# Kernel optimization log

Hardware: AMD Instinct MI355X
Metric: run time of the kernel (lower is better)

Reference implementation:

```python
import jax, jax.numpy as jnp
import numpy as np

B, T, M = 8, 4096, 1024
EPS = 1e-6
WINDOW = 15.0
INIT_GATE_BIAS = -3.0


def setup_inputs() -> dict:
    key = jax.random.key(0)
    k1, _ = jax.random.split(key)
    x = jax.random.normal(k1, (B, T, M), dtype=jnp.float32)
    # causal mask as in typical usage: lower-triangular (T, T)
    mask = jnp.tril(jnp.ones((T, T), dtype=jnp.float32))
    # learned gate parameter initialized to init_gate_bias
    gate_raw = jnp.full((M,), INIT_GATE_BIAS, dtype=jnp.float32)
    return {"x": x, "mask": mask, "gate_raw": gate_raw}


def _bump_kernel(T_len: int) -> jnp.ndarray:
    # K[i,j] convex bump in (i-j), supported on j in [i-window, i], K[i,i]=1
    i = jnp.arange(T_len, dtype=jnp.float32)[:, None]
    j = jnp.arange(T_len, dtype=jnp.float32)[None, :]
    diff = jnp.clip(i - j, 0.0, WINDOW)
    u = jnp.minimum(diff / WINDOW, 1.0 - EPS)
    K = jnp.exp(1.0 - 1.0 / (1.0 - u * u + EPS))
    K = jnp.where(i - j > WINDOW, 0.0, K)
    return K


def reference(x, mask, gate_raw):
    Bv, Tv, Mv = x.shape
    K = _bump_kernel(Tv).astype(x.dtype)
    K = K * mask.reshape(Tv, Tv).astype(x.dtype)
    K = K / jnp.maximum(K.sum(-1, keepdims=True), EPS)
    phi = jnp.einsum('ij,bjm->bim', K, x)  # (B, T, M)
    gate = jax.nn.softplus(gate_raw).reshape(1, 1, Mv)
    return phi * gate
```

## Files before the change

### kernel.cpp

```cpp
#include <hip/hip_runtime.h>
#include <math.h>

#define B_ 8
#define T_ 4096
#define M_ 1024
#define TT 64
#define EPSF 1e-6f

__global__ __launch_bounds__(256) void bump_conv_kernel(
    const float* __restrict__ x,
    const float* __restrict__ gate_raw,
    float* __restrict__ out) {
  const int tiles = T_ / TT;
  const int tile = blockIdx.x % tiles;
  const int b    = blockIdx.x / tiles;
  const int t0   = tile * TT;
  const int m    = threadIdx.x * 4;

  float w[16];
  float S = 0.0f;
#pragma unroll
  for (int d = 0; d < 16; ++d) {
    float u = fminf((float)d * (1.0f / 15.0f), 1.0f - EPSF);
    float den = 1.0f - u * u + EPSF;
    w[d] = expf(1.0f - 1.0f / den);
    S += w[d];
  }
  const float rsS = 1.0f / fmaxf(S, EPSF);

  const float4 graw = *(const float4*)(gate_raw + m);
  float4 g;
  g.x = fmaxf(graw.x, 0.0f) + log1pf(expf(-fabsf(graw.x)));
  g.y = fmaxf(graw.y, 0.0f) + log1pf(expf(-fabsf(graw.y)));
  g.z = fmaxf(graw.z, 0.0f) + log1pf(expf(-fabsf(graw.z)));
  g.w = fmaxf(graw.w, 0.0f) + log1pf(expf(-fabsf(graw.w)));

  const float* xb = x   + (size_t)b * T_ * M_ + m;
  float*       ob = out + (size_t)b * T_ * M_ + m;

  float4 r[16];
  r[0] = make_float4(0.f, 0.f, 0.f, 0.f);
#pragma unroll
  for (int k = 1; k <= 15; ++k) {
    const int t = t0 - 16 + k;
    r[k] = (t >= 0) ? *(const float4*)(xb + (size_t)t * M_)
                    : make_float4(0.f, 0.f, 0.f, 0.f);
  }
  float4 nxt = *(const float4*)(xb + (size_t)t0 * M_);

  for (int c = 0; c < TT / 16; ++c) {
#pragma unroll
    for (int s = 0; s < 16; ++s) {
      const int t = t0 + c * 16 + s;
      const float4 cur = nxt;
      const int tn = t + 1;
      if (tn < T_) nxt = *(const float4*)(xb + (size_t)tn * M_);
      r[s] = cur;

      float ax = 0.f, ay = 0.f, az = 0.f, aw = 0.f;
#pragma unroll
      for (int d = 0; d < 16; ++d) {
        const float4 v = r[(s - d + 16) & 15];
        const float wd = w[d];
        ax = fmaf(wd, v.x, ax);
        ay = fmaf(wd, v.y, ay);
        az = fmaf(wd, v.z, az);
        aw = fmaf(wd, v.w, aw);
      }

      float sc = rsS;
      if (t < 15) {
        float p = 0.0f;
#pragma unroll
        for (int d = 0; d < 16; ++d) p += (d <= t) ? w[d] : 0.0f;
        sc = 1.0f / fmaxf(p, EPSF);
      }

      float4 o;
      o.x = ax * sc * g.x;
      o.y = ay * sc * g.y;
      o.z = az * sc * g.z;
      o.w = aw * sc * g.w;
      *(float4*)(ob + (size_t)t * M_) = o;
    }
  }
}

extern "C" void kernel_launch(void* const* d_in, const int* in_sizes, int n_in,
                              void* d_out, int out_size, void* d_ws, size_t ws_size,
                              hipStream_t stream) {
  const float* x         = (const float*)d_in[0];
  const float* gate_raw  = (const float*)d_in[2];
  float*       out       = (float*)d_out;

  dim3 grid(B_ * (T_ / TT));
  dim3 block(256);
  bump_conv_kernel<<<grid, block, 0, stream>>>(x, gate_raw, out);
}
```

Before: 266.3 us.

## Compute 16-row output groups per block with batched register-buffered loads

Restructures the convolution so each block produces 16 time steps from 31 input rows, loaded in batches of eight into register buffers and scattered into 16 accumulators. This replaces the serial one-row-ahead prefetch over a 64-row tile, increasing loads in flight and the number of blocks. It trades this for roughly doubled halo reads per output, which rely on cache hits, and higher register pressure.

```diff
diff --git a/kernel.cpp b/kernel.cpp
--- a/kernel.cpp
+++ b/kernel.cpp
@@ -4,17 +4,18 @@
 #define B_ 8
 #define T_ 4096
 #define M_ 1024
-#define TT 64
+#define G_ 16
+#define R_ 31
 #define EPSF 1e-6f
 
 __global__ __launch_bounds__(256) void bump_conv_kernel(
     const float* __restrict__ x,
     const float* __restrict__ gate_raw,
     float* __restrict__ out) {
-  const int tiles = T_ / TT;
-  const int tile = blockIdx.x % tiles;
-  const int b    = blockIdx.x / tiles;
-  const int t0   = tile * TT;
+  const int groups = T_ / G_;
+  const int grp  = blockIdx.x % groups;
+  const int b    = blockIdx.x / groups;
+  const int base = grp * G_;
   const int m    = threadIdx.x * 4;
 
   float w[16];
@@ -38,62 +39,77 @@
   const float* xb = x   + (size_t)b * T_ * M_ + m;
   float*       ob = out + (size_t)b * T_ * M_ + m;
 
-  float4 r[16];
-  r[0] = make_float4(0.f, 0.f, 0.f, 0.f);
+  float4 acc[G_];
 #pragma unroll
-  for (int k = 1; k <= 15; ++k) {
-    const int t = t0 - 16 + k;
-    r[k] = (t >= 0) ? *(const float4*)(xb + (size_t)t * M_)
-                    : make_float4(0.f, 0.f, 0.f, 0.f);
+  for (int s = 0; s < G_; ++s) acc[s] = make_float4(0.f, 0.f, 0.f, 0.f);
+
+#define LOADJ(j) \
+  ((base - 15 + (j)) >= 0 ? *(const float4*)(xb + (size_t)(base - 15 + (j)) * M_) \
+                          : make_float4(0.f, 0.f, 0.f, 0.f))
+
+#define ACCJ(j, v)                                                   \
+  do {                                                               \
+    _Pragma("unroll")                                                \
+    for (int s = 0; s < G_; ++s) {                                   \
+      if (s >= (j) - 15 && s <= (j)) {                               \
+        const float wd = w[s + 15 - (j)];                            \
+        acc[s].x = fmaf(wd, (v).x, acc[s].x);                        \
+        acc[s].y = fmaf(wd, (v).y, acc[s].y);                        \
+        acc[s].z = fmaf(wd, (v).z, acc[s].z);                        \
+        acc[s].w = fmaf(wd, (v).w, acc[s].w);                        \
+      }                                                              \
+    }                                                                \
+  } while (0)
+
+  float4 bufA[8], bufB[8];
+#pragma unroll
+  for (int i = 0; i < 8; ++i) bufA[i] = LOADJ(i);
+#pragma unroll
+  for (int i = 0; i < 8; ++i) bufB[i] = LOADJ(8 + i);
+
+#pragma unroll
+  for (int i = 0; i < 8; ++i) ACCJ(i, bufA[i]);
+#pragma unroll
+  for (int i = 0; i < 8; ++i) bufA[i] = *(const float4*)(xb + (size_t)(base + 1 + i) * M_);
+
+#pragma unroll
+  for (int i = 0; i < 8; ++i) ACCJ(8 + i, bufB[i]);
+#pragma unroll
+  for (int i = 0; i < 7; ++i) bufB[i] = *(const float4*)(xb + (size_t)(base + 9 + i) * M_);
+
+#pragma unroll
+  for (int i = 0; i < 8; ++i) ACCJ(16 + i, bufA[i]);
+#pragma unroll
+  for (int i = 0; i < 7; ++i) ACCJ(24 + i, bufB[i]);
+
+#pragma unroll
+  for (int s = 0; s < G_; ++s) {
+    float sc = rsS;
+    if (s < 15 && base == 0) {
+      float p = 0.0f;
+#pragma unroll
+      for (int d = 0; d < 16; ++d) p += (d <= s) ? w[d] : 0.0f;
+      sc = 1.0f / fmaxf(p, EPSF);
+    }
+    float4 o;
+    o.x = acc[s].x * sc * g.x;
+    o.y = acc[s].y * sc * g.y;
+    o.z = acc[s].z * sc * g.z;
+    o.w = acc[s].w * sc * g.w;
+    *(float4*)(ob + (size_t)(base + s) * M_) = o;
   }
-  float4 nxt = *(const float4*)(xb + (size_t)t0 * M_);
-
-  for (int c = 0; c < TT / 16; ++c) {
-#pragma unroll
-    for (int s = 0; s < 16; ++s) {
-      const int t = t0 + c * 16 + s;
-      const float4 cur = nxt;
-      const int tn = t + 1;
-      if (tn < T_) nxt = *(const float4*)(xb + (size_t)tn * M_);
-      r[s] = cur;
-
-      float ax = 0.f, ay = 0.f, az = 0.f, aw = 0.f;
-#pragma unroll
-      for (int d = 0; d < 16; ++d) {
-        const float4 v = r[(s - d + 16) & 15];
-        const float wd = w[d];
-        ax = fmaf(wd, v.x, ax);
-        ay = fmaf(wd, v.y, ay);
-        az = fmaf(wd, v.z, az);
-        aw = fmaf(wd, v.w, aw);
-      }
-
-      float sc = rsS;
-      if (t < 15) {
-        float p = 0.0f;
-#pragma unroll
-        for (int d = 0; d < 16; ++d) p += (d <= t) ? w[d] : 0.0f;
-        sc = 1.0f / fmaxf(p, EPSF);
-      }
-
-      float4 o;
-      o.x = ax * sc * g.x;
-      o.y = ay * sc * g.y;
-      o.z = az * sc * g.z;
-      o.w = aw * sc * g.w;
-      *(float4*)(ob + (size_t)t * M_) = o;
-    }
-  }
+#undef LOADJ
+#undef ACCJ
 }
 
 extern "C" void kernel_launch(void* const* d_in, const int* in_sizes, int n_in,
                               void* d_out, int out_size, void* d_ws, size_t ws_size,
                               hipStream_t stream) {
-  const float* x         = (const float*)d_in[0];
-  const float* gate_raw  = (const float*)d_in[2];
-  float*       out       = (float*)d_out;
+  const float* x        = (const float*)d_in[0];
+  const float* gate_raw = (const float*)d_in[2];
+  float*       out      = (float*)d_out;
 
-  dim3 grid(B_ * (T_ / TT));
+  dim3 grid(B_ * (T_ / G_));
   dim3 block(256);
   bump_conv_kernel<<<grid, block, 0, stream>>>(x, gate_raw, out);
 }
```

Measured after the change: 267.2 us. Within noise of the previous version (+0.3%).
